# Kernel tuning notes

Hardware: AMD Instinct MI355X
Metric: run time of the kernel (lower is better)

Reference implementation:

```python
import jax, jax.numpy as jnp
import numpy as np

N_NODES = 15
EMBED_DIM = 2048
F1 = 1024
F2 = 512
N_EDGES = 120


def gcn_conv(x, src, dst, W, b):
    # PyG GCNConv: h = D^{-1/2} (A + I) D^{-1/2} (x W) + b
    h = x @ W                                   # [N, F_out]
    n = h.shape[0]
    loops = jnp.arange(n)
    s = jnp.concatenate([src, loops])
    d = jnp.concatenate([dst, loops])
    deg = jax.ops.segment_sum(jnp.ones_like(d, dtype=h.dtype), d, num_segments=n)
    dinv = jax.lax.rsqrt(deg)                   # deg >= 1 due to self loops
    norm = dinv[s] * dinv[d]                    # [E+N]
    out = jax.ops.segment_sum(h[s] * norm[:, None], d, num_segments=n)
    return out + b


def attention_pool(x, attW):
    # SimGNN-style attention: global ctx = tanh(mean(x W)); scores = sigmoid(x @ ctx)
    ctx = jnp.tanh(jnp.mean(x @ attW, axis=0))  # [F2]
    scores = jax.nn.sigmoid(x @ ctx)            # [N]
    return x.T @ scores                         # [F2]


def setup_inputs() -> dict:
    key = jax.random.key(0)
    ks = jax.random.split(key, 16)
    d = {}
    d['features_1'] = jax.random.normal(ks[0], (N_NODES,), dtype=jnp.float32)
    d['edge_index_1'] = jax.random.randint(ks[1], (2, N_EDGES), 0, N_NODES, dtype=jnp.int32)
    d['target'] = jax.random.uniform(ks[2], (3,), dtype=jnp.float32)
    def lin(k, fi, fo):
        s = 1.0 / np.sqrt(fi)
        kw, kb = jax.random.split(k)
        return (jax.random.uniform(kw, (fi, fo), minval=-s, maxval=s, dtype=jnp.float32),
                jax.random.uniform(kb, (fo,), minval=-s, maxval=s, dtype=jnp.float32))
    d['W1'], d['b1'] = lin(ks[3], 15, 15 * 32)
    d['W2'], d['b2'] = lin(ks[4], 15 * 32, 15 * 128)
    d['W3'], d['b3'] = lin(ks[5], 15 * 128, 15 * EMBED_DIM)
    d['gW1'], d['gb1'] = lin(ks[6], EMBED_DIM, F1)
    d['gW2'], d['gb2'] = lin(ks[7], F1, F2)
    d['attW'] = jax.random.normal(ks[8], (F2, F2), dtype=jnp.float32) * (1.0 / np.sqrt(F2))
    d['fcW'], d['fcb'] = lin(ks[9], F2, 3)
    return d


def reference(features_1, edge_index_1, target, W1, b1, W2, b2, W3, b3,
              gW1, gb1, gW2, gb2, attW, fcW, fcb):
    # embed MLP: 15 -> 480 -> 1920 -> 15*embed_dim
    h = jax.nn.relu(features_1 @ W1 + b1)
    h = jax.nn.relu(h @ W2 + b2)
    h = (h @ W3 + b3).reshape(N_NODES, EMBED_DIM)
    src, dst = edge_index_1[0], edge_index_1[1]
    x = jax.nn.relu(gcn_conv(h, src, dst, gW1, gb1))
    x = gcn_conv(x, src, dst, gW2, gb2)
    rep = attention_pool(x, attW)               # [F2]
    logits = rep @ fcW + fcb                    # [3]
    cls = jnp.argmax(target)
    loss = -jax.nn.log_softmax(logits)[cls]
    predictions = jax.nn.softmax(logits)
    return loss, predictions
```

## Files before the change

### kernel.cpp

```cpp
#include <hip/hip_runtime.h>
#include <math.h>

#define NN 15
#define EMBED 2048
#define F1D 1024
#define F2D 512
#define NE 120
#define H1_DIM 480
#define H2_DIM 1920
#define H3_DIM 30720

#define OFF_A    0
#define OFF_H2   256
#define OFF_P3   2304
#define OFF_XG1  493824
#define OFF_P1   524544
#define OFF_XG2  770304
#define OFF_P2   785664
#define OFF_X2   908544
#define OFF_XBAR 916224
#define OFF_CTX  916736

typedef float vf4 __attribute__((ext_vector_type(4)));

__device__ inline void f4ma(float4& a, float s, const float4& w) {
    a.x += s * w.x; a.y += s * w.y; a.z += s * w.z; a.w += s * w.w;
}
__device__ inline void f4acc(float4& a, const float4& b) {
    a.x += b.x; a.y += b.y; a.z += b.z; a.w += b.w;
}

__global__ void k1_h2(const float* __restrict__ f, const float* __restrict__ W1,
                      const float* __restrict__ b1, const float* __restrict__ W2,
                      const float* __restrict__ b2, const int* __restrict__ edges,
                      float* __restrict__ ws) {
    int tid = threadIdx.x;
    if (blockIdx.x == 60) {
        __shared__ float dinv[NN];
        __shared__ float A[NN * NN];
        if (tid < NN) {
            int deg = 1;
            for (int i = 0; i < NE; ++i) deg += (edges[NE + i] == tid) ? 1 : 0;
            dinv[tid] = rsqrtf((float)deg);
        }
        __syncthreads();
        if (tid < NN * NN) {
            int r = tid / NN, c = tid % NN;
            A[tid] = (r == c) ? dinv[r] * dinv[r] : 0.0f;
        }
        __syncthreads();
        if (tid == 0) {
            for (int i = 0; i < NE; ++i) {
                int s = edges[i], d = edges[NE + i];
                A[d * NN + s] += dinv[s] * dinv[d];
            }
        }
        __syncthreads();
        if (tid < NN * NN) ws[OFF_A + tid] = A[tid];
        return;
    }
    __shared__ float h1[H1_DIM];
    __shared__ float4 red[32][8];
    float fr[NN];
#pragma unroll
    for (int k = 0; k < NN; ++k) fr[k] = f[k];
    for (int j = tid; j < H1_DIM; j += 256) {
        float acc = b1[j];
#pragma unroll
        for (int k = 0; k < NN; ++k) acc += fr[k] * W1[k * H1_DIM + j];
        h1[j] = fmaxf(acc, 0.0f);
    }
    __syncthreads();
    int jg = tid & 7, kc = tid >> 3;
    int j = blockIdx.x * 32 + jg * 4;
    float4 acc = make_float4(0.f, 0.f, 0.f, 0.f);
    for (int r = 0; r < 15; ++r) {
        int k = kc * 15 + r;
        float4 w = *(const float4*)(W2 + k * H2_DIM + j);
        f4ma(acc, h1[k], w);
    }
    red[kc][jg] = acc;
    __syncthreads();
    for (int s = 16; s >= 1; s >>= 1) {
        if (kc < s) f4acc(red[kc][jg], red[kc + s][jg]);
        __syncthreads();
    }
    if (kc == 0) {
        float4 b = *(const float4*)(b2 + j);
        float4 v = red[0][jg];
        v.x = fmaxf(v.x + b.x, 0.f); v.y = fmaxf(v.y + b.y, 0.f);
        v.z = fmaxf(v.z + b.z, 0.f); v.w = fmaxf(v.w + b.w, 0.f);
        *(float4*)(ws + OFF_H2 + j) = v;
    }
}

__global__ void k2_h3(const float* __restrict__ W3, float* __restrict__ ws) {
    __shared__ float cval[120];
    __shared__ int   coff[120];
    __shared__ int   wcnt[2];
    int tid = threadIdx.x;
    int cb = blockIdx.x, kc = blockIdx.y;
    int kbase = kc * 120;
    float hv = 0.0f;
    if (tid < 120) hv = ws[OFF_H2 + kbase + tid];
    int lane = tid & 63, wv = tid >> 6;
    bool act = (tid < 120) && (hv != 0.0f);
    unsigned long long m = __ballot(act);
    if (wv < 2 && lane == 0) wcnt[wv] = __popcll(m);
    __syncthreads();
    if (act) {
        int off = (wv == 1) ? wcnt[0] : 0;
        int p = off + __popcll(m & ((1ull << lane) - 1ull));
        coff[p] = (kbase + tid) * H3_DIM;
        cval[p] = hv;
    }
    __syncthreads();
    int nr = wcnt[0] + wcnt[1];
    if (tid >= 240) return;
    int col = cb * 960 + tid * 4;
    float4 acc = make_float4(0.f, 0.f, 0.f, 0.f);
#pragma unroll 8
    for (int r = 0; r < nr; ++r) {
        vf4 w = __builtin_nontemporal_load((const vf4*)(W3 + (size_t)coff[r] + col));
        float s = cval[r];
        acc.x += s * w.x; acc.y += s * w.y; acc.z += s * w.z; acc.w += s * w.w;
    }
    *(float4*)(ws + OFF_P3 + (size_t)kc * H3_DIM + col) = acc;
}

__global__ void k3_agg1(const float* __restrict__ b3, float* __restrict__ ws) {
    __shared__ float Al[NN * NN];
    __shared__ float S[NN][32];
    int tid = threadIdx.x;
    int c0 = blockIdx.x * 32;
    for (int i = tid; i < NN * NN; i += 256) Al[i] = ws[OFF_A + i];
    for (int q = tid; q < NN * 32; q += 256) {
        int m = q >> 5, c = q & 31;
        int j = m * EMBED + c0 + c;
        float s = b3[j];
#pragma unroll
        for (int p = 0; p < 16; ++p) s += ws[OFF_P3 + p * H3_DIM + j];
        S[m][c] = s;
    }
    __syncthreads();
    for (int q = tid; q < NN * 32; q += 256) {
        int n = q >> 5, c = q & 31;
        float x = 0.f;
#pragma unroll
        for (int m = 0; m < NN; ++m) x += Al[n * NN + m] * S[m][c];
        ws[OFF_XG1 + n * EMBED + c0 + c] = x;
    }
}

template<int IN, int OUT, int ECH>
__global__ void k_mmP(const float* __restrict__ X, const float* __restrict__ W,
                      float* __restrict__ P) {
    __shared__ float Xl[NN * ECH];
    __shared__ float4 red[8][32][NN];
    int tid = threadIdx.x;
    int e0 = blockIdx.y * ECH;
    for (int i = tid; i < NN * ECH; i += 256) {
        int n = i / ECH, e = i - n * ECH;
        Xl[i] = X[n * IN + e0 + e];
    }
    __syncthreads();
    int fg = tid & 31, kt = tid >> 5;
    int f = blockIdx.x * 128 + fg * 4;
    float4 acc[NN];
#pragma unroll
    for (int n = 0; n < NN; ++n) acc[n] = make_float4(0.f, 0.f, 0.f, 0.f);
    const int RPT = ECH / 8;
    for (int r = 0; r < RPT; ++r) {
        int e = kt * RPT + r;
        float4 w = *(const float4*)(W + (size_t)(e0 + e) * OUT + f);
#pragma unroll
        for (int n = 0; n < NN; ++n) f4ma(acc[n], Xl[n * ECH + e], w);
    }
    __syncthreads();
#pragma unroll
    for (int n = 0; n < NN; ++n) red[kt][fg][n] = acc[n];
    __syncthreads();
    for (int s = 4; s >= 1; s >>= 1) {
        if (kt < s) {
#pragma unroll
            for (int n = 0; n < NN; ++n) f4acc(red[kt][fg][n], red[kt + s][fg][n]);
        }
        __syncthreads();
    }
    if (kt == 0) {
#pragma unroll
        for (int n = 0; n < NN; ++n) {
            float4 v = red[0][fg][n];
            *(float4*)(P + (size_t)blockIdx.y * NN * OUT + n * OUT + f) = v;
        }
    }
}

__global__ void k5_fin1(const float* __restrict__ gb1, float* __restrict__ ws) {
    __shared__ float Al[NN * NN];
    __shared__ float S[NN][64];
    int tid = threadIdx.x;
    int f0 = blockIdx.x * 64;
    for (int i = tid; i < NN * NN; i += 256) Al[i] = ws[OFF_A + i];
    for (int q = tid; q < NN * 64; q += 256) {
        int n = q >> 6, c = q & 63;
        float s = gb1[f0 + c];
#pragma unroll
        for (int p = 0; p < 16; ++p) s += ws[OFF_P1 + p * (NN * F1D) + n * F1D + f0 + c];
        S[n][c] = fmaxf(s, 0.f);
    }
    __syncthreads();
    for (int q = tid; q < NN * 64; q += 256) {
        int n = q >> 6, c = q & 63;
        float x = 0.f;
#pragma unroll
        for (int m = 0; m < NN; ++m) x += Al[n * NN + m] * S[m][c];
        ws[OFF_XG2 + n * F1D + f0 + c] = x;
    }
}

__global__ void k7_fin2(const float* __restrict__ gb2, float* __restrict__ ws) {
    __shared__ float S[NN][64];
    int tid = threadIdx.x;
    int f0 = blockIdx.x * 64;
    for (int q = tid; q < NN * 64; q += 256) {
        int n = q >> 6, c = q & 63;
        float s = gb2[f0 + c];
#pragma unroll
        for (int p = 0; p < 16; ++p) s += ws[OFF_P2 + p * (NN * F2D) + n * F2D + f0 + c];
        S[n][c] = s;
        ws[OFF_X2 + n * F2D + f0 + c] = s;
    }
    __syncthreads();
    if (tid < 64) {
        float s = 0.f;
#pragma unroll
        for (int n = 0; n < NN; ++n) s += S[n][tid];
        ws[OFF_XBAR + f0 + tid] = s * (1.0f / 15.0f);
    }
}

__global__ void k8_ctx(const float* __restrict__ attW, float* __restrict__ ws) {
    __shared__ float xb[F2D];
    __shared__ float4 red[64][4];
    int tid = threadIdx.x;
    for (int e = tid; e < F2D; e += 256) xb[e] = ws[OFF_XBAR + e];
    __syncthreads();
    int fg = tid & 3, kt = tid >> 2;
    int f = blockIdx.x * 16 + fg * 4;
    float4 acc = make_float4(0.f, 0.f, 0.f, 0.f);
    for (int r = 0; r < 8; ++r) {
        int e = kt * 8 + r;
        float4 w = *(const float4*)(attW + e * F2D + f);
        f4ma(acc, xb[e], w);
    }
    red[kt][fg] = acc;
    __syncthreads();
    for (int s = 32; s >= 1; s >>= 1) {
        if (kt < s) f4acc(red[kt][fg], red[kt + s][fg]);
        __syncthreads();
    }
    if (kt == 0) {
        float4 v = red[0][fg];
        ws[OFF_CTX + f + 0] = tanhf(v.x);
        ws[OFF_CTX + f + 1] = tanhf(v.y);
        ws[OFF_CTX + f + 2] = tanhf(v.z);
        ws[OFF_CTX + f + 3] = tanhf(v.w);
    }
}

__global__ void k9_final(const float* __restrict__ fcW, const float* __restrict__ fcb,
                         const float* __restrict__ target, const float* __restrict__ ws,
                         float* __restrict__ out) {
    __shared__ float x2l[NN * F2D];
    __shared__ float ctxl[F2D];
    __shared__ float scores[16];
    __shared__ float rep[F2D];
    __shared__ float logits[3];
    int tid = threadIdx.x;
    for (int i = tid; i < NN * F2D; i += 256) x2l[i] = ws[OFF_X2 + i];
    for (int i = tid; i < F2D; i += 256) ctxl[i] = ws[OFF_CTX + i];
    __syncthreads();
    {
        int g = tid >> 4, l = tid & 15;
        if (g < NN) {
            float p = 0.f;
            for (int i = 0; i < 32; ++i) {
                int e = l + 16 * i;
                p += x2l[g * F2D + e] * ctxl[e];
            }
            p += __shfl_xor(p, 1); p += __shfl_xor(p, 2);
            p += __shfl_xor(p, 4); p += __shfl_xor(p, 8);
            if (l == 0) scores[g] = 1.0f / (1.0f + expf(-p));
        }
    }
    __syncthreads();
    for (int fi = tid; fi < F2D; fi += 256) {
        float v = 0.f;
#pragma unroll
        for (int n = 0; n < NN; ++n) v += x2l[n * F2D + fi] * scores[n];
        rep[fi] = v;
    }
    __syncthreads();
    if (tid < 192) {
        int j = tid >> 6, l = tid & 63;
        float p = 0.f;
        for (int i = 0; i < 8; ++i) {
            int e = l + 64 * i;
            p += rep[e] * fcW[e * 3 + j];
        }
        p += __shfl_xor(p, 1); p += __shfl_xor(p, 2); p += __shfl_xor(p, 4);
        p += __shfl_xor(p, 8); p += __shfl_xor(p, 16); p += __shfl_xor(p, 32);
        if (l == 0) logits[j] = p + fcb[j];
    }
    __syncthreads();
    if (tid == 0) {
        float t0 = target[0], t1 = target[1], t2 = target[2];
        int cls = 0; float best = t0;
        if (t1 > best) { best = t1; cls = 1; }
        if (t2 > best) { cls = 2; }
        float l0 = logits[0], l1 = logits[1], l2 = logits[2];
        float m = fmaxf(l0, fmaxf(l1, l2));
        float e0 = expf(l0 - m), e1 = expf(l1 - m), e2 = expf(l2 - m);
        float s = e0 + e1 + e2;
        float lc = (cls == 0) ? l0 : ((cls == 1) ? l1 : l2);
        out[0] = -(lc - m - logf(s));
        out[1] = e0 / s; out[2] = e1 / s; out[3] = e2 / s;
    }
}

extern "C" void kernel_launch(void* const* d_in, const int* in_sizes, int n_in,
                              void* d_out, int out_size, void* d_ws, size_t ws_size,
                              hipStream_t stream) {
    const float* f    = (const float*)d_in[0];
    const int*   ei   = (const int*)d_in[1];
    const float* tgt  = (const float*)d_in[2];
    const float* W1   = (const float*)d_in[3];
    const float* b1   = (const float*)d_in[4];
    const float* W2   = (const float*)d_in[5];
    const float* b2   = (const float*)d_in[6];
    const float* W3   = (const float*)d_in[7];
    const float* b3   = (const float*)d_in[8];
    const float* gW1  = (const float*)d_in[9];
    const float* gb1  = (const float*)d_in[10];
    const float* gW2  = (const float*)d_in[11];
    const float* gb2  = (const float*)d_in[12];
    const float* attW = (const float*)d_in[13];
    const float* fcW  = (const float*)d_in[14];
    const float* fcb  = (const float*)d_in[15];
    float* ws  = (float*)d_ws;
    float* out = (float*)d_out;

    k1_h2<<<dim3(61), dim3(256), 0, stream>>>(f, W1, b1, W2, b2, ei, ws);
    k2_h3<<<dim3(32, 16), dim3(256), 0, stream>>>(W3, ws);
    k3_agg1<<<dim3(64), dim3(256), 0, stream>>>(b3, ws);
    k_mmP<2048, 1024, 128><<<dim3(8, 16), dim3(256), 0, stream>>>(ws + OFF_XG1, gW1, ws + OFF_P1);
    k5_fin1<<<dim3(16), dim3(256), 0, stream>>>(gb1, ws);
    k_mmP<1024, 512, 64><<<dim3(4, 16), dim3(256), 0, stream>>>(ws + OFF_XG2, gW2, ws + OFF_P2);
    k7_fin2<<<dim3(8), dim3(256), 0, stream>>>(gb2, ws);
    k8_ctx<<<dim3(32), dim3(256), 0, stream>>>(attW, ws);
    k9_final<<<dim3(1), dim3(256), 0, stream>>>(fcW, fcb, tgt, ws, out);
}
```

Baseline: 375.2 us.

## Fuse GCN tail stages into one cooperative persistent kernel with grid syncs

Replaces seven small kernel launches (aggregation, two GCN matmuls, finalizers, context, final head) with a single cooperative kernel of 256 blocks that steps through the stages separated by grid-wide barriers. It also re-partitions the work: the gW1 matmul now splits the reduction dimension into 32 chunks instead of 16, and the aggregation steps use finer column slices per block. The aim is to remove launch overhead and inter-kernel gaps. In exchange it pays for grid.sync barriers and leaves many blocks idle in the later stages.

```diff
diff --git a/kernel.cpp b/kernel.cpp
--- a/kernel.cpp
+++ b/kernel.cpp
@@ -1,5 +1,8 @@
 #include <hip/hip_runtime.h>
+#include <hip/hip_cooperative_groups.h>
 #include <math.h>
+
+namespace cg = cooperative_groups;
 
 #define NN 15
 #define EMBED 2048
@@ -15,11 +18,11 @@
 #define OFF_P3   2304
 #define OFF_XG1  493824
 #define OFF_P1   524544
-#define OFF_XG2  770304
-#define OFF_P2   785664
-#define OFF_X2   908544
-#define OFF_XBAR 916224
-#define OFF_CTX  916736
+#define OFF_XG2  1016064
+#define OFF_P2   1031424
+#define OFF_X2   1154304
+#define OFF_XBAR 1161984
+#define OFF_CTX  1162496
 
 typedef float vf4 __attribute__((ext_vector_type(4)));
 
@@ -128,204 +131,249 @@
     *(float4*)(ws + OFF_P3 + (size_t)kc * H3_DIM + col) = acc;
 }
 
-__global__ void k3_agg1(const float* __restrict__ b3, float* __restrict__ ws) {
-    __shared__ float Al[NN * NN];
-    __shared__ float S[NN][32];
+__global__ void __launch_bounds__(256, 1)
+k_tail(const float* __restrict__ b3, const float* __restrict__ gW1,
+       const float* __restrict__ gb1, const float* __restrict__ gW2,
+       const float* __restrict__ gb2, const float* __restrict__ attW,
+       const float* __restrict__ fcW, const float* __restrict__ fcb,
+       const float* __restrict__ target, float* __restrict__ ws,
+       float* __restrict__ out) {
+    cg::grid_group grid = cg::this_grid();
+    __shared__ float4 red4[8][32][NN];
+    __shared__ float Xl[NN * 64];
+    __shared__ float Al[240];
+    float* Sf = (float*)red4;
     int tid = threadIdx.x;
-    int c0 = blockIdx.x * 32;
+    int b = blockIdx.x;
+
     for (int i = tid; i < NN * NN; i += 256) Al[i] = ws[OFF_A + i];
-    for (int q = tid; q < NN * 32; q += 256) {
-        int m = q >> 5, c = q & 31;
-        int j = m * EMBED + c0 + c;
-        float s = b3[j];
-#pragma unroll
-        for (int p = 0; p < 16; ++p) s += ws[OFF_P3 + p * H3_DIM + j];
-        S[m][c] = s;
-    }
-    __syncthreads();
-    for (int q = tid; q < NN * 32; q += 256) {
-        int n = q >> 5, c = q & 31;
-        float x = 0.f;
-#pragma unroll
-        for (int m = 0; m < NN; ++m) x += Al[n * NN + m] * S[m][c];
-        ws[OFF_XG1 + n * EMBED + c0 + c] = x;
-    }
-}
-
-template<int IN, int OUT, int ECH>
-__global__ void k_mmP(const float* __restrict__ X, const float* __restrict__ W,
-                      float* __restrict__ P) {
-    __shared__ float Xl[NN * ECH];
-    __shared__ float4 red[8][32][NN];
-    int tid = threadIdx.x;
-    int e0 = blockIdx.y * ECH;
-    for (int i = tid; i < NN * ECH; i += 256) {
-        int n = i / ECH, e = i - n * ECH;
-        Xl[i] = X[n * IN + e0 + e];
-    }
-    __syncthreads();
-    int fg = tid & 31, kt = tid >> 5;
-    int f = blockIdx.x * 128 + fg * 4;
-    float4 acc[NN];
-#pragma unroll
-    for (int n = 0; n < NN; ++n) acc[n] = make_float4(0.f, 0.f, 0.f, 0.f);
-    const int RPT = ECH / 8;
-    for (int r = 0; r < RPT; ++r) {
-        int e = kt * RPT + r;
-        float4 w = *(const float4*)(W + (size_t)(e0 + e) * OUT + f);
-#pragma unroll
-        for (int n = 0; n < NN; ++n) f4ma(acc[n], Xl[n * ECH + e], w);
-    }
-    __syncthreads();
-#pragma unroll
-    for (int n = 0; n < NN; ++n) red[kt][fg][n] = acc[n];
-    __syncthreads();
-    for (int s = 4; s >= 1; s >>= 1) {
-        if (kt < s) {
-#pragma unroll
-            for (int n = 0; n < NN; ++n) f4acc(red[kt][fg][n], red[kt + s][fg][n]);
-        }
-        __syncthreads();
-    }
-    if (kt == 0) {
-#pragma unroll
-        for (int n = 0; n < NN; ++n) {
-            float4 v = red[0][fg][n];
-            *(float4*)(P + (size_t)blockIdx.y * NN * OUT + n * OUT + f) = v;
-        }
-    }
-}
-
-__global__ void k5_fin1(const float* __restrict__ gb1, float* __restrict__ ws) {
-    __shared__ float Al[NN * NN];
-    __shared__ float S[NN][64];
-    int tid = threadIdx.x;
-    int f0 = blockIdx.x * 64;
-    for (int i = tid; i < NN * NN; i += 256) Al[i] = ws[OFF_A + i];
-    for (int q = tid; q < NN * 64; q += 256) {
-        int n = q >> 6, c = q & 63;
-        float s = gb1[f0 + c];
-#pragma unroll
-        for (int p = 0; p < 16; ++p) s += ws[OFF_P1 + p * (NN * F1D) + n * F1D + f0 + c];
-        S[n][c] = fmaxf(s, 0.f);
-    }
-    __syncthreads();
-    for (int q = tid; q < NN * 64; q += 256) {
-        int n = q >> 6, c = q & 63;
-        float x = 0.f;
-#pragma unroll
-        for (int m = 0; m < NN; ++m) x += Al[n * NN + m] * S[m][c];
-        ws[OFF_XG2 + n * F1D + f0 + c] = x;
-    }
-}
-
-__global__ void k7_fin2(const float* __restrict__ gb2, float* __restrict__ ws) {
-    __shared__ float S[NN][64];
-    int tid = threadIdx.x;
-    int f0 = blockIdx.x * 64;
-    for (int q = tid; q < NN * 64; q += 256) {
-        int n = q >> 6, c = q & 63;
-        float s = gb2[f0 + c];
-#pragma unroll
-        for (int p = 0; p < 16; ++p) s += ws[OFF_P2 + p * (NN * F2D) + n * F2D + f0 + c];
-        S[n][c] = s;
-        ws[OFF_X2 + n * F2D + f0 + c] = s;
-    }
-    __syncthreads();
-    if (tid < 64) {
-        float s = 0.f;
-#pragma unroll
-        for (int n = 0; n < NN; ++n) s += S[n][tid];
-        ws[OFF_XBAR + f0 + tid] = s * (1.0f / 15.0f);
-    }
-}
-
-__global__ void k8_ctx(const float* __restrict__ attW, float* __restrict__ ws) {
-    __shared__ float xb[F2D];
-    __shared__ float4 red[64][4];
-    int tid = threadIdx.x;
-    for (int e = tid; e < F2D; e += 256) xb[e] = ws[OFF_XBAR + e];
-    __syncthreads();
-    int fg = tid & 3, kt = tid >> 2;
-    int f = blockIdx.x * 16 + fg * 4;
-    float4 acc = make_float4(0.f, 0.f, 0.f, 0.f);
-    for (int r = 0; r < 8; ++r) {
-        int e = kt * 8 + r;
-        float4 w = *(const float4*)(attW + e * F2D + f);
-        f4ma(acc, xb[e], w);
-    }
-    red[kt][fg] = acc;
-    __syncthreads();
-    for (int s = 32; s >= 1; s >>= 1) {
-        if (kt < s) f4acc(red[kt][fg], red[kt + s][fg]);
-        __syncthreads();
-    }
-    if (kt == 0) {
-        float4 v = red[0][fg];
-        ws[OFF_CTX + f + 0] = tanhf(v.x);
-        ws[OFF_CTX + f + 1] = tanhf(v.y);
-        ws[OFF_CTX + f + 2] = tanhf(v.z);
-        ws[OFF_CTX + f + 3] = tanhf(v.w);
-    }
-}
-
-__global__ void k9_final(const float* __restrict__ fcW, const float* __restrict__ fcb,
-                         const float* __restrict__ target, const float* __restrict__ ws,
-                         float* __restrict__ out) {
-    __shared__ float x2l[NN * F2D];
-    __shared__ float ctxl[F2D];
-    __shared__ float scores[16];
-    __shared__ float rep[F2D];
-    __shared__ float logits[3];
-    int tid = threadIdx.x;
-    for (int i = tid; i < NN * F2D; i += 256) x2l[i] = ws[OFF_X2 + i];
-    for (int i = tid; i < F2D; i += 256) ctxl[i] = ws[OFF_CTX + i];
-    __syncthreads();
+
     {
-        int g = tid >> 4, l = tid & 15;
-        if (g < NN) {
+        int c0 = b * 8;
+        if (tid < 120) {
+            int mm = tid >> 3, c = tid & 7;
+            int j = mm * EMBED + c0 + c;
+            float s = b3[j];
+#pragma unroll
+            for (int p = 0; p < 16; ++p) s += ws[OFF_P3 + p * H3_DIM + j];
+            Sf[mm * 8 + c] = s;
+        }
+        __syncthreads();
+        if (tid < 120) {
+            int n = tid >> 3, c = tid & 7;
+            float x = 0.f;
+#pragma unroll
+            for (int mm = 0; mm < NN; ++mm) x += Al[n * NN + mm] * Sf[mm * 8 + c];
+            ws[OFF_XG1 + n * EMBED + c0 + c] = x;
+        }
+    }
+    __threadfence();
+    grid.sync();
+
+    {
+        int e0 = (b & 31) * 64;
+        for (int i = tid; i < NN * 64; i += 256) {
+            int n = i >> 6, e = i & 63;
+            Xl[i] = ws[OFF_XG1 + n * EMBED + e0 + e];
+        }
+        __syncthreads();
+        int fg = tid & 31, kt = tid >> 5;
+        int fcol = (b >> 5) * 128 + fg * 4;
+        float4 acc[NN];
+#pragma unroll
+        for (int n = 0; n < NN; ++n) acc[n] = make_float4(0.f, 0.f, 0.f, 0.f);
+        for (int r = 0; r < 8; ++r) {
+            int e = kt * 8 + r;
+            float4 w = *(const float4*)(gW1 + (size_t)(e0 + e) * F1D + fcol);
+#pragma unroll
+            for (int n = 0; n < NN; ++n) f4ma(acc[n], Xl[n * 64 + e], w);
+        }
+        __syncthreads();
+#pragma unroll
+        for (int n = 0; n < NN; ++n) red4[kt][fg][n] = acc[n];
+        __syncthreads();
+        for (int s = 4; s >= 1; s >>= 1) {
+            if (kt < s) {
+#pragma unroll
+                for (int n = 0; n < NN; ++n) f4acc(red4[kt][fg][n], red4[kt + s][fg][n]);
+            }
+            __syncthreads();
+        }
+        if (kt == 0) {
+#pragma unroll
+            for (int n = 0; n < NN; ++n)
+                *(float4*)(ws + OFF_P1 + (size_t)(b & 31) * (NN * F1D) + n * F1D + fcol) = red4[0][fg][n];
+        }
+    }
+    __threadfence();
+    grid.sync();
+
+    {
+        int c0 = b * 4;
+        if (tid < 60) {
+            int mm = tid >> 2, c = tid & 3;
+            float s = gb1[c0 + c];
+#pragma unroll
+            for (int p = 0; p < 32; ++p) s += ws[OFF_P1 + p * (NN * F1D) + mm * F1D + c0 + c];
+            Sf[mm * 4 + c] = fmaxf(s, 0.f);
+        }
+        __syncthreads();
+        if (tid < 60) {
+            int n = tid >> 2, c = tid & 3;
+            float x = 0.f;
+#pragma unroll
+            for (int mm = 0; mm < NN; ++mm) x += Al[n * NN + mm] * Sf[mm * 4 + c];
+            ws[OFF_XG2 + n * F1D + c0 + c] = x;
+        }
+    }
+    __threadfence();
+    grid.sync();
+
+    if (b < 64) {
+        int e0 = (b & 15) * 64;
+        for (int i = tid; i < NN * 64; i += 256) {
+            int n = i >> 6, e = i & 63;
+            Xl[i] = ws[OFF_XG2 + n * F1D + e0 + e];
+        }
+        __syncthreads();
+        int fg = tid & 31, kt = tid >> 5;
+        int fcol = (b >> 4) * 128 + fg * 4;
+        float4 acc[NN];
+#pragma unroll
+        for (int n = 0; n < NN; ++n) acc[n] = make_float4(0.f, 0.f, 0.f, 0.f);
+        for (int r = 0; r < 8; ++r) {
+            int e = kt * 8 + r;
+            float4 w = *(const float4*)(gW2 + (size_t)(e0 + e) * F2D + fcol);
+#pragma unroll
+            for (int n = 0; n < NN; ++n) f4ma(acc[n], Xl[n * 64 + e], w);
+        }
+        __syncthreads();
+#pragma unroll
+        for (int n = 0; n < NN; ++n) red4[kt][fg][n] = acc[n];
+        __syncthreads();
+        for (int s = 4; s >= 1; s >>= 1) {
+            if (kt < s) {
+#pragma unroll
+                for (int n = 0; n < NN; ++n) f4acc(red4[kt][fg][n], red4[kt + s][fg][n]);
+            }
+            __syncthreads();
+        }
+        if (kt == 0) {
+#pragma unroll
+            for (int n = 0; n < NN; ++n)
+                *(float4*)(ws + OFF_P2 + (size_t)(b & 15) * (NN * F2D) + n * F2D + fcol) = red4[0][fg][n];
+        }
+    }
+    __threadfence();
+    grid.sync();
+
+    {
+        int c0 = b * 2;
+        if (tid < 30) {
+            int mm = tid >> 1, c = tid & 1;
+            float s = gb2[c0 + c];
+#pragma unroll
+            for (int p = 0; p < 16; ++p) s += ws[OFF_P2 + p * (NN * F2D) + mm * F2D + c0 + c];
+            ws[OFF_X2 + mm * F2D + c0 + c] = s;
+            Sf[tid] = s;
+        }
+        __syncthreads();
+        if (tid < 2) {
+            float s = 0.f;
+#pragma unroll
+            for (int n = 0; n < NN; ++n) s += Sf[n * 2 + tid];
+            ws[OFF_XBAR + c0 + tid] = s * (1.0f / 15.0f);
+        }
+    }
+    __threadfence();
+    grid.sync();
+
+    if (b < 32) {
+        float* xb = Sf;
+        float4* redc = (float4*)(Sf + 512);
+        for (int e = tid; e < F2D; e += 256) xb[e] = ws[OFF_XBAR + e];
+        __syncthreads();
+        int fg = tid & 3, kt = tid >> 2;
+        int fcol = b * 16 + fg * 4;
+        float4 acc = make_float4(0.f, 0.f, 0.f, 0.f);
+        for (int r = 0; r < 8; ++r) {
+            int e = kt * 8 + r;
+            float4 w = *(const float4*)(attW + e * F2D + fcol);
+            f4ma(acc, xb[e], w);
+        }
+        redc[kt * 4 + fg] = acc;
+        __syncthreads();
+        for (int s = 32; s >= 1; s >>= 1) {
+            if (kt < s) f4acc(redc[kt * 4 + fg], redc[(kt + s) * 4 + fg]);
+            __syncthreads();
+        }
+        if (kt == 0) {
+            float4 v = redc[fg];
+            ws[OFF_CTX + fcol + 0] = tanhf(v.x);
+            ws[OFF_CTX + fcol + 1] = tanhf(v.y);
+            ws[OFF_CTX + fcol + 2] = tanhf(v.z);
+            ws[OFF_CTX + fcol + 3] = tanhf(v.w);
+        }
+    }
+    __threadfence();
+    grid.sync();
+
+    if (b != 0) return;
+    {
+        float* x2l   = Sf;
+        float* ctxl  = Sf + 7680;
+        float* scores= Sf + 8192;
+        float* rep   = Sf + 8208;
+        float* logit = Sf + 8720;
+        for (int i = tid; i < NN * F2D; i += 256) x2l[i] = ws[OFF_X2 + i];
+        for (int i = tid; i < F2D; i += 256) ctxl[i] = ws[OFF_CTX + i];
+        __syncthreads();
+        {
+            int g = tid >> 4, l = tid & 15;
+            if (g < NN) {
+                float p = 0.f;
+                for (int i = 0; i < 32; ++i) {
+                    int e = l + 16 * i;
+                    p += x2l[g * F2D + e] * ctxl[e];
+                }
+                p += __shfl_xor(p, 1); p += __shfl_xor(p, 2);
+                p += __shfl_xor(p, 4); p += __shfl_xor(p, 8);
+                if (l == 0) scores[g] = 1.0f / (1.0f + expf(-p));
+            }
+        }
+        __syncthreads();
+        for (int fi = tid; fi < F2D; fi += 256) {
+            float v = 0.f;
+#pragma unroll
+            for (int n = 0; n < NN; ++n) v += x2l[n * F2D + fi] * scores[n];
+            rep[fi] = v;
+        }
+        __syncthreads();
+        if (tid < 192) {
+            int j = tid >> 6, l = tid & 63;
             float p = 0.f;
-            for (int i = 0; i < 32; ++i) {
-                int e = l + 16 * i;
-                p += x2l[g * F2D + e] * ctxl[e];
+            for (int i = 0; i < 8; ++i) {
+                int e = l + 64 * i;
+                p += rep[e] * fcW[e * 3 + j];
             }
-            p += __shfl_xor(p, 1); p += __shfl_xor(p, 2);
-            p += __shfl_xor(p, 4); p += __shfl_xor(p, 8);
-            if (l == 0) scores[g] = 1.0f / (1.0f + expf(-p));
-        }
-    }
-    __syncthreads();
-    for (int fi = tid; fi < F2D; fi += 256) {
-        float v = 0.f;
-#pragma unroll
-        for (int n = 0; n < NN; ++n) v += x2l[n * F2D + fi] * scores[n];
-        rep[fi] = v;
-    }
-    __syncthreads();
-    if (tid < 192) {
-        int j = tid >> 6, l = tid & 63;
-        float p = 0.f;
-        for (int i = 0; i < 8; ++i) {
-            int e = l + 64 * i;
-            p += rep[e] * fcW[e * 3 + j];
-        }
-        p += __shfl_xor(p, 1); p += __shfl_xor(p, 2); p += __shfl_xor(p, 4);
-        p += __shfl_xor(p, 8); p += __shfl_xor(p, 16); p += __shfl_xor(p, 32);
-        if (l == 0) logits[j] = p + fcb[j];
-    }
-    __syncthreads();
-    if (tid == 0) {
-        float t0 = target[0], t1 = target[1], t2 = target[2];
-        int cls = 0; float best = t0;
-        if (t1 > best) { best = t1; cls = 1; }
-        if (t2 > best) { cls = 2; }
-        float l0 = logits[0], l1 = logits[1], l2 = logits[2];
-        float m = fmaxf(l0, fmaxf(l1, l2));
-        float e0 = expf(l0 - m), e1 = expf(l1 - m), e2 = expf(l2 - m);
-        float s = e0 + e1 + e2;
-        float lc = (cls == 0) ? l0 : ((cls == 1) ? l1 : l2);
-        out[0] = -(lc - m - logf(s));
-        out[1] = e0 / s; out[2] = e1 / s; out[3] = e2 / s;
+            p += __shfl_xor(p, 1); p += __shfl_xor(p, 2); p += __shfl_xor(p, 4);
+            p += __shfl_xor(p, 8); p += __shfl_xor(p, 16); p += __shfl_xor(p, 32);
+            if (l == 0) logit[j] = p + fcb[j];
+        }
+        __syncthreads();
+        if (tid == 0) {
+            float t0 = target[0], t1 = target[1], t2 = target[2];
+            int cls = 0; float best = t0;
+            if (t1 > best) { best = t1; cls = 1; }
+            if (t2 > best) { cls = 2; }
+            float l0 = logit[0], l1 = logit[1], l2 = logit[2];
+            float mx = fmaxf(l0, fmaxf(l1, l2));
+            float e0 = expf(l0 - mx), e1 = expf(l1 - mx), e2 = expf(l2 - mx);
+            float s = e0 + e1 + e2;
+            float lc = (cls == 0) ? l0 : ((cls == 1) ? l1 : l2);
+            out[0] = -(lc - mx - logf(s));
+            out[1] = e0 / s; out[2] = e1 / s; out[3] = e2 / s;
+        }
     }
 }
 
@@ -353,11 +401,9 @@
 
     k1_h2<<<dim3(61), dim3(256), 0, stream>>>(f, W1, b1, W2, b2, ei, ws);
     k2_h3<<<dim3(32, 16), dim3(256), 0, stream>>>(W3, ws);
-    k3_agg1<<<dim3(64), dim3(256), 0, stream>>>(b3, ws);
-    k_mmP<2048, 1024, 128><<<dim3(8, 16), dim3(256), 0, stream>>>(ws + OFF_XG1, gW1, ws + OFF_P1);
-    k5_fin1<<<dim3(16), dim3(256), 0, stream>>>(gb1, ws);
-    k_mmP<1024, 512, 64><<<dim3(4, 16), dim3(256), 0, stream>>>(ws + OFF_XG2, gW2, ws + OFF_P2);
-    k7_fin2<<<dim3(8), dim3(256), 0, stream>>>(gb2, ws);
-    k8_ctx<<<dim3(32), dim3(256), 0, stream>>>(attW, ws);
-    k9_final<<<dim3(1), dim3(256), 0, stream>>>(fcW, fcb, tgt, ws, out);
-}
+
+    void* args[] = {(void*)&b3, (void*)&gW1, (void*)&gb1, (void*)&gW2, (void*)&gb2,
+                    (void*)&attW, (void*)&fcW, (void*)&fcb, (void*)&tgt,
+                    (void*)&ws, (void*)&out};
+    hipLaunchCooperativeKernel((const void*)k_tail, dim3(256), dim3(256), args, 0, stream);
+}
```

Measured after the change: 676.1 us. 1.8x slower.
